# Kernel tuning notes

Hardware: AMD Instinct MI355X
Metric: run time of the kernel (lower is better)

## Reference

```python
import jax, jax.numpy as jnp
import numpy as np

BETA = 25.0  # torch nn.Softplus(beta=25.0)

def softplus_b(z):
    return jax.nn.softplus(BETA * z) / BETA

def setup_inputs() -> dict:
    key = jax.random.key(0)
    ks = jax.random.split(key, 9)
    B, H = 16384, 512
    def lin_init(kw, kb, out_f, in_f):
        bound = 1.0 / np.sqrt(in_f)
        W = jax.random.uniform(kw, (out_f, in_f), jnp.float32, -bound, bound)
        b = jax.random.uniform(kb, (out_f,), jnp.float32, -bound, bound)
        return W, b
    W0, b0 = lin_init(ks[1], ks[2], H, 4)
    W1, b1 = lin_init(ks[3], ks[4], H, H)
    W2, b2 = lin_init(ks[5], ks[6], H, H)
    W3, b3 = lin_init(ks[7], ks[8], 5, H)
    x = jax.random.normal(ks[0], (B, 4), jnp.float32)
    return {"x": x, "W0": W0, "b0": b0, "W1": W1, "b1": b1,
            "W2": W2, "b2": b2, "W3": W3, "b3": b3}

def reference(x, W0, b0, W1, b1, W2, b2, W3, b3):
    def net(z):  # (4,) -> (5,)
        h = softplus_b(W0 @ z + b0)
        h = softplus_b(W1 @ h + b1)
        h = softplus_b(W2 @ h + b2)
        return W3 @ h + b3

    def A_matrix(z):  # antisymmetrized Jacobian of first 4 outputs, (4,4)
        J = jax.jacrev(lambda p: net(p)[:4])(z)
        return J - J.T

    def point_trace(z):
        # T[i,j,k] = d A[i,j] / d z[k]; torch einsum('...ii') -> sum_j T[i,j,j]
        T = jax.jacfwd(A_matrix)(z)  # (4,4,4)
        return jnp.einsum('ijj->i', T)  # (4,)

    trace = jax.vmap(point_trace)(x)          # (B,4)
    u = jax.vmap(net)(x)                      # (B,5)
    return jnp.concatenate([trace, u[:, 4:5]], axis=1)  # (B,5)
```

## Files before the change

### kernel.cpp

```cpp
#include <hip/hip_runtime.h>
#include <math.h>

#define HDIM 512
#define NCH 16
#define BETA 25.0f
#define KV 1536
#define NKH 48

typedef unsigned short ushort_t;
typedef __attribute__((ext_vector_type(8))) short short8;
typedef __attribute__((ext_vector_type(4))) float f32x4;

__device__ __forceinline__ ushort_t f2bf(float f) {
    unsigned u = __float_as_uint(f);
    unsigned r = (u + 0x7fff + ((u >> 16) & 1)) >> 16;
    return (ushort_t)r;
}
__device__ __forceinline__ float bf2f(ushort_t b) {
    return __uint_as_float(((unsigned)b) << 16);
}
__device__ __forceinline__ void split_bf(float v, ushort_t& hi, ushort_t& lo) {
    hi = f2bf(v);
    lo = f2bf(v - bf2f(hi));
}

__device__ __forceinline__ void softplus_jet(float v, float& phi, float& s, float& pp) {
    float y = BETA * v;
    float e = expf(-fabsf(y));
    float inv = 1.0f / (1.0f + e);
    s = (y >= 0.0f) ? inv : e * inv;
    phi = (fmaxf(y, 0.0f) + log1pf(e)) * (1.0f / BETA);
    pp = BETA * s * (1.0f - s);
}

__device__ __forceinline__ void gl_lds16(const void* g, void* l) {
    __builtin_amdgcn_global_load_lds(
        (const __attribute__((address_space(1))) unsigned int*)g,
        (__attribute__((address_space(3))) unsigned int*)l, 16, 0, 0);
}

__global__ __launch_bounds__(256) void layer0_jet(
    const float* __restrict__ x, const float* __restrict__ W0,
    const float* __restrict__ b0, ushort_t* __restrict__ A0)
{
    __shared__ ushort_t sm[16 * 1024];
    int p = blockIdx.x, tid = threadIdx.x;
    float4 z = *reinterpret_cast<const float4*>(&x[p * 4]);
#pragma unroll
    for (int half = 0; half < 2; ++half) {
        int n = half * 256 + tid;
        float4 w = *reinterpret_cast<const float4*>(&W0[n * 4]);
        float v = fmaf(w.x, z.x, fmaf(w.y, z.y, fmaf(w.z, z.z, fmaf(w.w, z.w, b0[n]))));
        float phi, s, pp;
        softplus_jet(v, phi, s, pp);
        float wa[4] = {w.x, w.y, w.z, w.w};
        float o[16];
        o[0] = phi;
#pragma unroll
        for (int a = 0; a < 4; ++a) o[1 + a] = s * wa[a];
        int idx = 5;
#pragma unroll
        for (int a = 0; a < 4; ++a)
#pragma unroll
            for (int b = a; b < 4; ++b) { o[idx] = pp * wa[a] * wa[b]; ++idx; }
        o[15] = 0.0f;
#pragma unroll
        for (int c = 0; c < 16; ++c) {
            ushort_t hb, lb;
            split_bf(o[c], hb, lb);
            sm[c * 1024 + n] = hb;
            sm[c * 1024 + 512 + n] = lb;
        }
    }
    __syncthreads();
    uint4* d4 = reinterpret_cast<uint4*>(A0 + (size_t)p * 16 * 1024);
    const uint4* s4 = reinterpret_cast<const uint4*>(sm);
#pragma unroll
    for (int i = 0; i < 8; ++i) d4[tid + 256 * i] = s4[tid + 256 * i];
}

template<int EPI>
__global__ __launch_bounds__(512, 2) void gemm_jet8(
    const ushort_t* __restrict__ Ag, const ushort_t* __restrict__ BT,
    const float* __restrict__ bias, ushort_t* __restrict__ Anext,
    float* __restrict__ Sout)
{
    __shared__ char smem[131072];
    ushort_t* Asl = (ushort_t*)smem;
    ushort_t* Bsl = (ushort_t*)(smem + 65536);
    float*    epi = (float*)smem;

    const int tid = threadIdx.x;
    const int wave = tid >> 6, lane = tid & 63;
    const int wr = wave >> 2, wc = wave & 3;

    int nwg = gridDim.x, bid = blockIdx.x;
    int q = nwg >> 3, r = nwg & 7;
    int xcd = bid & 7, i8 = bid >> 3;
    int logical = (xcd < r ? xcd * (q + 1) : r * (q + 1) + (xcd - r) * q) + i8;
    const int mt = logical >> 1;
    const int m0 = mt * 256;
    const int n0 = (logical & 1) * 256;

    const int s_w2 = wave * 2;
    const int s_r  = lane >> 2;
    const int s_c  = (lane & 3) * 8;

    f32x4 acc[8][4] = {};

    auto stageA = [&](int g) {
        if (g >= NKH) g -= NKH;
        const int slot = g & 3;
        int k0 = g * 32;
        int ka = (k0 < 512) ? k0 : k0 - 512;
#pragma unroll
        for (int rr = 0; rr < 2; ++rr) {
            int row = (s_w2 + rr) * 16 + s_r;
            gl_lds16(Ag + (size_t)(m0 + row) * 1024 + ka + s_c,
                     Asl + slot * 8192 + (s_w2 + rr) * 512);
        }
    };
    auto stageB = [&](int g) {
        if (g >= NKH) g -= NKH;
        const int slot = g & 3;
        int k0 = g * 32;
#pragma unroll
        for (int rr = 0; rr < 2; ++rr) {
            int row = (s_w2 + rr) * 16 + s_r;
            gl_lds16(BT + (size_t)(n0 + row) * KV + k0 + s_c,
                     Bsl + slot * 8192 + (s_w2 + rr) * 512);
        }
    };

    stageA(0); stageB(0); stageA(1); stageB(1); stageA(2); stageB(2);
    asm volatile("s_waitcnt vmcnt(8)" ::: "memory");
    __builtin_amdgcn_s_barrier();
    asm volatile("" ::: "memory");

    const int rA = lane & 15;
    const int kc = (lane >> 4) * 8;

    for (int j = 0; j < 12; ++j) {
        short8 bf[4];
#pragma unroll
        for (int p = 0; p < 8; ++p) {
            const int kh = p >> 1, qm = p & 1;
            const int slot = kh;
            const ushort_t* Ab = Asl + slot * 8192;
            const ushort_t* Bb = Bsl + slot * 8192;
            short8 af[4];
#pragma unroll
            for (int mi = 0; mi < 4; ++mi)
                af[mi] = *(const short8*)&Ab[(wr * 128 + qm * 64 + mi * 16 + rA) * 32 + kc];
            if (qm == 0) {
#pragma unroll
                for (int ni = 0; ni < 4; ++ni)
                    bf[ni] = *(const short8*)&Bb[(wc * 64 + ni * 16 + rA) * 32 + kc];
            }
            if (qm == 0) stageA(4 * j + 3 + kh); else stageB(4 * j + 3 + kh);
            if (qm == 1) asm volatile("s_waitcnt vmcnt(8)" ::: "memory");
            asm volatile("" ::: "memory");
            __builtin_amdgcn_s_barrier();
            asm volatile("s_waitcnt lgkmcnt(0)" ::: "memory");
            __builtin_amdgcn_sched_barrier(0);
            __builtin_amdgcn_s_setprio(1);
#pragma unroll
            for (int mi = 0; mi < 4; ++mi)
#pragma unroll
                for (int ni = 0; ni < 4; ++ni)
                    acc[qm * 4 + mi][ni] = __builtin_amdgcn_mfma_f32_16x16x32_bf16(
                        af[mi], bf[ni], acc[qm * 4 + mi][ni], 0, 0, 0);
            __builtin_amdgcn_s_setprio(0);
            asm volatile("" ::: "memory");
            __builtin_amdgcn_s_barrier();
            asm volatile("" ::: "memory");
        }
    }

    asm volatile("s_waitcnt vmcnt(0)" ::: "memory");
    __builtin_amdgcn_s_barrier();
    asm volatile("" ::: "memory");

    const int pl = lane & 15, ph = lane >> 4;
#pragma unroll
    for (int h = 0; h < 2; ++h) {
        if (h) { asm volatile("" ::: "memory"); __builtin_amdgcn_s_barrier(); }
        if (wr == h) {
#pragma unroll
            for (int am = 0; am < 8; ++am)
#pragma unroll
                for (int ni = 0; ni < 4; ++ni)
#pragma unroll
                    for (int rr = 0; rr < 4; ++rr)
                        epi[(am * 16 + ph * 4 + rr) * 256 + wc * 64 + ni * 16 + pl] = acc[am][ni][rr];
        }
        asm volatile("" ::: "memory");
        __builtin_amdgcn_s_barrier();
        asm volatile("" ::: "memory");
#pragma unroll
        for (int rep = 0; rep < 4; ++rep) {
            int idx = rep * 512 + tid;
            int n = idx & 255, pq = idx >> 8;
            const float* vp = &epi[pq * 16 * 256 + n];
            float v[15];
#pragma unroll
            for (int c = 0; c < 15; ++c) v[c] = vp[c * 256];
            float val = v[0] + bias[n0 + n];
            float phi, s, pp;
            softplus_jet(val, phi, s, pp);
            float o[16];
            o[0] = phi;
            float d[4];
#pragma unroll
            for (int a = 0; a < 4; ++a) { d[a] = v[1 + a]; o[1 + a] = s * d[a]; }
            int ix = 5;
#pragma unroll
            for (int a = 0; a < 4; ++a)
#pragma unroll
                for (int b = a; b < 4; ++b) { o[ix] = pp * d[a] * d[b] + s * v[ix]; ++ix; }
            o[15] = 0.0f;
            size_t prow = (size_t)mt * 16 + h * 8 + pq;
            if (EPI == 1) {
                size_t rb = prow * 16 * 1024;
#pragma unroll
                for (int c = 0; c < 16; ++c) {
                    ushort_t hb, lb;
                    split_bf(o[c], hb, lb);
                    Anext[rb + (size_t)c * 1024 + n0 + n] = hb;
                    Anext[rb + (size_t)c * 1024 + 512 + n0 + n] = lb;
                }
            } else {
                float4* op = reinterpret_cast<float4*>(Sout + ((size_t)prow * 512 + n0 + n) * 16);
#pragma unroll
                for (int qq = 0; qq < 4; ++qq)
                    op[qq] = make_float4(o[4*qq], o[4*qq+1], o[4*qq+2], o[4*qq+3]);
            }
        }
    }
}

__global__ __launch_bounds__(256) void trace_kernel(
    const float* __restrict__ Sin, const float* __restrict__ W3,
    const float* __restrict__ b3, float* __restrict__ out, int npts)
{
    int wave = threadIdx.x >> 6;
    int lane = threadIdx.x & 63;
    int p = blockIdx.x * 4 + wave;
    if (p >= npts) return;
    const float* sp = Sin + (size_t)p * (HDIM * NCH);

    float hu[4][10];
#pragma unroll
    for (int m = 0; m < 4; ++m)
#pragma unroll
        for (int qq = 0; qq < 10; ++qq) hu[m][qq] = 0.0f;
    float u4 = 0.0f;

    for (int kk = 0; kk < 8; ++kk) {
        int k = kk * 64 + lane;
        const float* sk = sp + k * NCH;
        float4 s0 = *reinterpret_cast<const float4*>(&sk[0]);
        float4 s1 = *reinterpret_cast<const float4*>(&sk[4]);
        float4 s2 = *reinterpret_cast<const float4*>(&sk[8]);
        float4 s3 = *reinterpret_cast<const float4*>(&sk[12]);
        float hv[10] = {s1.y,s1.z,s1.w, s2.x,s2.y,s2.z,s2.w, s3.x,s3.y,s3.z};
        float w3m[5];
#pragma unroll
        for (int m = 0; m < 5; ++m) w3m[m] = W3[m * HDIM + k];
        u4 = fmaf(w3m[4], s0.x, u4);
#pragma unroll
        for (int m = 0; m < 4; ++m)
#pragma unroll
            for (int qq = 0; qq < 10; ++qq) hu[m][qq] = fmaf(w3m[m], hv[qq], hu[m][qq]);
    }

#pragma unroll
    for (int off = 32; off > 0; off >>= 1) {
#pragma unroll
        for (int m = 0; m < 4; ++m)
#pragma unroll
            for (int qq = 0; qq < 10; ++qq) hu[m][qq] += __shfl_xor(hu[m][qq], off, 64);
        u4 += __shfl_xor(u4, off, 64);
    }

    if (lane == 0) {
        const int Pm[4][4] = {{0,1,2,3},{1,4,5,6},{2,5,7,8},{3,6,8,9}};
        const int Pd[4] = {0, 4, 7, 9};
#pragma unroll
        for (int i = 0; i < 4; ++i) {
            float t1 = hu[i][Pd[0]] + hu[i][Pd[1]] + hu[i][Pd[2]] + hu[i][Pd[3]];
            float t2 = hu[0][Pm[0][i]] + hu[1][Pm[1][i]] + hu[2][Pm[2][i]] + hu[3][Pm[3][i]];
            out[p * 5 + i] = t1 - t2;
        }
        out[p * 5 + 4] = u4 + b3[4];
    }
}

__global__ void prep_B(const float* __restrict__ W1, const float* __restrict__ W2,
                       ushort_t* __restrict__ BT1, ushort_t* __restrict__ BT2)
{
    int tid = blockIdx.x * 256 + threadIdx.x;
    int l = tid >> 18;
    int i = tid & 262143;
    int n = i >> 9, k = i & 511;
    const float* W = l ? W2 : W1;
    ushort_t* BT = l ? BT2 : BT1;
    float v = W[i];
    ushort_t hb, lb;
    split_bf(v, hb, lb);
    size_t rr = (size_t)n * KV;
    BT[rr + k] = hb;
    BT[rr + 512 + k] = lb;
    BT[rr + 1024 + k] = hb;
}

extern "C" void kernel_launch(void* const* d_in, const int* in_sizes, int n_in,
                              void* d_out, int out_size, void* d_ws, size_t ws_size,
                              hipStream_t stream)
{
    const float* x  = (const float*)d_in[0];
    const float* W0 = (const float*)d_in[1];
    const float* b0 = (const float*)d_in[2];
    const float* W1 = (const float*)d_in[3];
    const float* b1 = (const float*)d_in[4];
    const float* W2 = (const float*)d_in[5];
    const float* b2 = (const float*)d_in[6];
    const float* W3 = (const float*)d_in[7];
    const float* b3 = (const float*)d_in[8];
    float* out = (float*)d_out;

    int B = in_sizes[0] / 4;

    ushort_t* BT1 = (ushort_t*)d_ws;
    ushort_t* BT2 = BT1 + 512 * KV;
    char* bufbase = (char*)(BT2 + 512 * KV);

    size_t avail = ws_size - 2ull * 512 * KV * sizeof(ushort_t);
    size_t per_pt = 2ull * 32768;
    int Pc = (int)(avail / per_pt) & ~15;
    if (Pc > 16384) Pc = 16384;
    if (Pc < 16) Pc = 16;

    ushort_t* A0 = (ushort_t*)bufbase;
    ushort_t* A1 = (ushort_t*)(bufbase + (size_t)Pc * 32768);
    float* S2 = (float*)A0;

    prep_B<<<2048, 256, 0, stream>>>(W1, W2, BT1, BT2);

    for (int base = 0; base < B; base += Pc) {
        int np = (B - base < Pc) ? (B - base) : Pc;
        layer0_jet<<<np, 256, 0, stream>>>(x + (size_t)base * 4, W0, b0, A0);
        int nwg = (np / 16) * 2;
        gemm_jet8<1><<<nwg, 512, 0, stream>>>(A0, BT1, b1, A1, nullptr);
        gemm_jet8<2><<<nwg, 512, 0, stream>>>(A1, BT2, b2, nullptr, S2);
        trace_kernel<<<(np + 3) / 4, 256, 0, stream>>>(S2, W3, b3, out + (size_t)base * 5, np);
    }
}
```

Baseline: 1.391 ms.

## Swizzle LDS layouts and software-pipeline fragment loads in GEMM main loop

```diff
diff --git a/kernel.cpp b/kernel.cpp
--- a/kernel.cpp
+++ b/kernel.cpp
@@ -103,8 +103,8 @@
     const int n0 = (logical & 1) * 256;
 
     const int s_w2 = wave * 2;
-    const int s_r  = lane >> 2;
-    const int s_c  = (lane & 3) * 8;
+    const int s_row = lane >> 2;
+    const int s_c  = (((lane & 3) - ((lane >> 3) & 3)) & 3) * 8;
 
     f32x4 acc[8][4] = {};
 
@@ -115,7 +115,7 @@
         int ka = (k0 < 512) ? k0 : k0 - 512;
 #pragma unroll
         for (int rr = 0; rr < 2; ++rr) {
-            int row = (s_w2 + rr) * 16 + s_r;
+            int row = (s_w2 + rr) * 16 + s_row;
             gl_lds16(Ag + (size_t)(m0 + row) * 1024 + ka + s_c,
                      Asl + slot * 8192 + (s_w2 + rr) * 512);
         }
@@ -126,62 +126,81 @@
         int k0 = g * 32;
 #pragma unroll
         for (int rr = 0; rr < 2; ++rr) {
-            int row = (s_w2 + rr) * 16 + s_r;
+            int row = (s_w2 + rr) * 16 + s_row;
             gl_lds16(BT + (size_t)(n0 + row) * KV + k0 + s_c,
                      Bsl + slot * 8192 + (s_w2 + rr) * 512);
         }
     };
+
+    const int rA = lane & 15;
+    const int rd = rA * 32 + ((((lane >> 4) + (rA >> 1)) & 3) * 8);
 
     stageA(0); stageB(0); stageA(1); stageB(1); stageA(2); stageB(2);
     asm volatile("s_waitcnt vmcnt(8)" ::: "memory");
     __builtin_amdgcn_s_barrier();
     asm volatile("" ::: "memory");
 
-    const int rA = lane & 15;
-    const int kc = (lane >> 4) * 8;
-
-    for (int j = 0; j < 12; ++j) {
-        short8 bf[4];
-#pragma unroll
-        for (int p = 0; p < 8; ++p) {
-            const int kh = p >> 1, qm = p & 1;
-            const int slot = kh;
-            const ushort_t* Ab = Asl + slot * 8192;
-            const ushort_t* Bb = Bsl + slot * 8192;
-            short8 af[4];
+    short8 afA[4], afB[4], bfr[4];
+#pragma unroll
+    for (int mi = 0; mi < 4; ++mi)
+        afA[mi] = *(const short8*)&Asl[(wr * 128 + mi * 16) * 32 + rd];
+#pragma unroll
+    for (int ni = 0; ni < 4; ++ni)
+        bfr[ni] = *(const short8*)&Bsl[(wc * 64 + ni * 16) * 32 + rd];
+
+#pragma unroll 4
+    for (int g = 0; g < NKH; ++g) {
+        const int slot = g & 3;
+        const int slot1 = (g + 1) & 3;
+        {
 #pragma unroll
             for (int mi = 0; mi < 4; ++mi)
-                af[mi] = *(const short8*)&Ab[(wr * 128 + qm * 64 + mi * 16 + rA) * 32 + kc];
-            if (qm == 0) {
+                afB[mi] = *(const short8*)&Asl[slot * 8192 + (wr * 128 + 64 + mi * 16) * 32 + rd];
+            stageA(g + 3);
+            asm volatile("s_waitcnt vmcnt(6)" ::: "memory");
+            __builtin_amdgcn_s_barrier();
+            __builtin_amdgcn_s_setprio(1);
+#pragma unroll
+            for (int mi = 0; mi < 4; ++mi)
 #pragma unroll
                 for (int ni = 0; ni < 4; ++ni)
-                    bf[ni] = *(const short8*)&Bb[(wc * 64 + ni * 16 + rA) * 32 + kc];
-            }
-            if (qm == 0) stageA(4 * j + 3 + kh); else stageB(4 * j + 3 + kh);
-            if (qm == 1) asm volatile("s_waitcnt vmcnt(8)" ::: "memory");
-            asm volatile("" ::: "memory");
-            __builtin_amdgcn_s_barrier();
-            asm volatile("s_waitcnt lgkmcnt(0)" ::: "memory");
-            __builtin_amdgcn_sched_barrier(0);
-            __builtin_amdgcn_s_setprio(1);
-#pragma unroll
-            for (int mi = 0; mi < 4; ++mi)
-#pragma unroll
-                for (int ni = 0; ni < 4; ++ni)
-                    acc[qm * 4 + mi][ni] = __builtin_amdgcn_mfma_f32_16x16x32_bf16(
-                        af[mi], bf[ni], acc[qm * 4 + mi][ni], 0, 0, 0);
+                    acc[mi][ni] = __builtin_amdgcn_mfma_f32_16x16x32_bf16(
+                        afA[mi], bfr[ni], acc[mi][ni], 0, 0, 0);
             __builtin_amdgcn_s_setprio(0);
             asm volatile("" ::: "memory");
             __builtin_amdgcn_s_barrier();
             asm volatile("" ::: "memory");
         }
-    }
-
-    asm volatile("s_waitcnt vmcnt(0)" ::: "memory");
+        {
+#pragma unroll
+            for (int mi = 0; mi < 4; ++mi)
+                afA[mi] = *(const short8*)&Asl[slot1 * 8192 + (wr * 128 + mi * 16) * 32 + rd];
+            stageB(g + 3);
+            asm volatile("s_waitcnt vmcnt(6)" ::: "memory");
+            __builtin_amdgcn_s_barrier();
+            __builtin_amdgcn_s_setprio(1);
+#pragma unroll
+            for (int mi = 0; mi < 4; ++mi)
+#pragma unroll
+                for (int ni = 0; ni < 4; ++ni)
+                    acc[4 + mi][ni] = __builtin_amdgcn_mfma_f32_16x16x32_bf16(
+                        afB[mi], bfr[ni], acc[4 + mi][ni], 0, 0, 0);
+            __builtin_amdgcn_s_setprio(0);
+#pragma unroll
+            for (int ni = 0; ni < 4; ++ni)
+                bfr[ni] = *(const short8*)&Bsl[slot1 * 8192 + (wc * 64 + ni * 16) * 32 + rd];
+            asm volatile("" ::: "memory");
+            __builtin_amdgcn_s_barrier();
+            asm volatile("" ::: "memory");
+        }
+    }
+
+    asm volatile("s_waitcnt vmcnt(0) lgkmcnt(0)" ::: "memory");
     __builtin_amdgcn_s_barrier();
     asm volatile("" ::: "memory");
 
     const int pl = lane & 15, ph = lane >> 4;
+    const int wxor = (ph & 1) << 4;
 #pragma unroll
     for (int h = 0; h < 2; ++h) {
         if (h) { asm volatile("" ::: "memory"); __builtin_amdgcn_s_barrier(); }
@@ -192,7 +211,7 @@
                 for (int ni = 0; ni < 4; ++ni)
 #pragma unroll
                     for (int rr = 0; rr < 4; ++rr)
-                        epi[(am * 16 + ph * 4 + rr) * 256 + wc * 64 + ni * 16 + pl] = acc[am][ni][rr];
+                        epi[(am * 16 + ph * 4 + rr) * 256 + ((wc * 64 + ni * 16 + pl) ^ wxor)] = acc[am][ni][rr];
         }
         asm volatile("" ::: "memory");
         __builtin_amdgcn_s_barrier();
@@ -201,10 +220,10 @@
         for (int rep = 0; rep < 4; ++rep) {
             int idx = rep * 512 + tid;
             int n = idx & 255, pq = idx >> 8;
-            const float* vp = &epi[pq * 16 * 256 + n];
+            const float* vp = &epi[pq * 16 * 256];
             float v[15];
 #pragma unroll
-            for (int c = 0; c < 15; ++c) v[c] = vp[c * 256];
+            for (int c = 0; c < 15; ++c) v[c] = vp[c * 256 + (n ^ (((c >> 2) & 1) << 4))];
             float val = v[0] + bias[n0 + n];
             float phi, s, pp;
             softplus_jet(val, phi, s, pp);
```

Result: faster. 1.316 ms (-5.4%).
